# Kernel optimization log

Hardware: AMD Instinct MI355X
Metric: run time of the kernel (lower is better)

Reference implementation:

```python
import jax, jax.numpy as jnp
import numpy as np

EMBED = 1024
HEADS = 16
HEAD_DIM = EMBED // HEADS
HIDDEN = int(EMBED * 4.0)
EPS = 1e-6


def setup_inputs() -> dict:
    key = jax.random.key(0)
    ks = jax.random.split(key, 8)
    s = lambda fan_in: 1.0 / np.sqrt(fan_in)
    x = jax.random.normal(ks[0], (2, 2048, EMBED), dtype=jnp.float32)
    return {
        "x": x,
        "ln1_g": jnp.ones((EMBED,), jnp.float32),
        "ln1_b": jnp.zeros((EMBED,), jnp.float32),
        "w_qkv": jax.random.normal(ks[1], (EMBED, 3 * EMBED), jnp.float32) * s(EMBED),
        "b_qkv": jnp.zeros((3 * EMBED,), jnp.float32),
        "w_proj": jax.random.normal(ks[2], (EMBED, EMBED), jnp.float32) * s(EMBED),
        "b_proj": jnp.zeros((EMBED,), jnp.float32),
        "ln2_g": jnp.ones((EMBED,), jnp.float32),
        "ln2_b": jnp.zeros((EMBED,), jnp.float32),
        "w_fc1": jax.random.normal(ks[3], (EMBED, HIDDEN), jnp.float32) * s(EMBED),
        "b_fc1": jnp.zeros((HIDDEN,), jnp.float32),
        "w_fc2": jax.random.normal(ks[4], (HIDDEN, EMBED), jnp.float32) * s(HIDDEN),
        "b_fc2": jnp.zeros((EMBED,), jnp.float32),
    }


def _layernorm(x, g, b):
    mu = jnp.mean(x, axis=-1, keepdims=True)
    var = jnp.mean(jnp.square(x - mu), axis=-1, keepdims=True)
    return (x - mu) * jax.lax.rsqrt(var + EPS) * g + b


def _attention(x, w_qkv, b_qkv, w_proj, b_proj):
    B, N, C = x.shape
    qkv = x @ w_qkv + b_qkv                      # [B,N,3C]
    qkv = qkv.reshape(B, N, 3, HEADS, HEAD_DIM)
    q, k, v = (qkv[:, :, 0], qkv[:, :, 1], qkv[:, :, 2])  # [B,N,H,Dh]
    scale = HEAD_DIM ** -0.5
    attn = jnp.einsum('bnhd,bmhd->bhnm', q, k) * scale     # [B,H,N,N]
    attn = jax.nn.softmax(attn, axis=-1)
    out = jnp.einsum('bhnm,bmhd->bnhd', attn, v).reshape(B, N, C)
    return out @ w_proj + b_proj


def reference(x, ln1_g, ln1_b, w_qkv, b_qkv, w_proj, b_proj,
              ln2_g, ln2_b, w_fc1, b_fc1, w_fc2, b_fc2):
    x = x + _attention(_layernorm(x, ln1_g, ln1_b), w_qkv, b_qkv, w_proj, b_proj)
    h = _layernorm(x, ln2_g, ln2_b)
    h = jax.nn.gelu(h @ w_fc1 + b_fc1, approximate=False)
    x = x + (h @ w_fc2 + b_fc2)
    return x
```

## Files before the change

kernel.cpp:

```cpp
#include <hip/hip_runtime.h>
#include <hip/hip_bf16.h>
#include <math.h>

typedef __bf16 bf16x8 __attribute__((ext_vector_type(8)));
typedef __bf16 bf16x4 __attribute__((ext_vector_type(4)));
typedef unsigned short u16x8 __attribute__((ext_vector_type(8)));
typedef float f32x4 __attribute__((ext_vector_type(4)));

#define EP_QKV 0
#define EP_GELU 1
#define EP_RES 2

static __device__ __forceinline__ unsigned short f2bf(float x) {
  unsigned int u = __float_as_uint(x);
  unsigned int r = (u + 0x7fffu + ((u >> 16) & 1u)) >> 16;
  return (unsigned short)r;
}

static __device__ __forceinline__ unsigned int pkbf(float lo, float hi) {
  return __builtin_amdgcn_perm(__float_as_uint(hi), __float_as_uint(lo), 0x07060302);
}

static __device__ __forceinline__ void async16(const void* g, void* l) {
  __builtin_amdgcn_global_load_lds((__attribute__((address_space(1))) void*)g,
                                   (__attribute__((address_space(3))) void*)l, 16, 0, 0);
}

__global__ __launch_bounds__(256) void wt_all(
    const float* __restrict__ i0, unsigned short* __restrict__ o0,
    const float* __restrict__ i1, unsigned short* __restrict__ o1,
    const float* __restrict__ i2, unsigned short* __restrict__ o2,
    const float* __restrict__ i3, unsigned short* __restrict__ o3) {
  __shared__ float tile[32][33];
  const int b = blockIdx.x;
  const float* in; unsigned short* out; int K, N, nbx, lb;
  if (b < 3072)      { in = i0; out = o0; K = 1024; N = 3072; nbx = 96;  lb = b; }
  else if (b < 4096) { in = i1; out = o1; K = 1024; N = 1024; nbx = 32;  lb = b - 3072; }
  else if (b < 8192) { in = i2; out = o2; K = 1024; N = 4096; nbx = 128; lb = b - 4096; }
  else               { in = i3; out = o3; K = 4096; N = 1024; nbx = 32;  lb = b - 8192; }
  const int n0 = (lb % nbx) * 32;
  const int k0 = (lb / nbx) * 32;
  const int tx = threadIdx.x;
  const int ty = threadIdx.y;
  #pragma unroll
  for (int i = ty; i < 32; i += 8)
    tile[i][tx] = in[(size_t)(k0 + i) * N + n0 + tx];
  __syncthreads();
  #pragma unroll
  for (int i = ty; i < 32; i += 8)
    out[(size_t)(n0 + i) * K + k0 + tx] = f2bf(tile[tx][i]);
}

__global__ __launch_bounds__(256) void ln_kernel(const float* __restrict__ x,
                                                 const float* __restrict__ g,
                                                 const float* __restrict__ b,
                                                 unsigned short* __restrict__ outp) {
  const int row = blockIdx.x;
  const int tid = threadIdx.x;
  const int wave = tid >> 6, lane = tid & 63;
  const float4 v = ((const float4*)(x + (size_t)row * 1024))[tid];
  float s = v.x + v.y + v.z + v.w;
  #pragma unroll
  for (int i = 1; i < 64; i <<= 1) s += __shfl_xor(s, i);
  __shared__ float red[4];
  if (lane == 0) red[wave] = s;
  __syncthreads();
  const float mean = (red[0] + red[1] + red[2] + red[3]) * (1.f / 1024.f);
  const float dx = v.x - mean, dy = v.y - mean, dz = v.z - mean, dw = v.w - mean;
  float ss = dx * dx + dy * dy + dz * dz + dw * dw;
  #pragma unroll
  for (int i = 1; i < 64; i <<= 1) ss += __shfl_xor(ss, i);
  __syncthreads();
  if (lane == 0) red[wave] = ss;
  __syncthreads();
  const float var = (red[0] + red[1] + red[2] + red[3]) * (1.f / 1024.f);
  const float inv = rsqrtf(var + 1e-6f);
  const float4 gv = ((const float4*)g)[tid];
  const float4 bv = ((const float4*)b)[tid];
  ushort4 o;
  o.x = f2bf(dx * inv * gv.x + bv.x);
  o.y = f2bf(dy * inv * gv.y + bv.y);
  o.z = f2bf(dz * inv * gv.z + bv.z);
  o.w = f2bf(dw * inv * gv.w + bv.w);
  ((ushort4*)(outp + (size_t)row * 1024))[tid] = o;
}

template <int TN, int BK, bool DBUF, int MODE, int MINW>
__global__ __launch_bounds__(256, MINW) void gemm_kernel(
    const unsigned short* __restrict__ A,
    const unsigned short* __restrict__ BT,
    const float* __restrict__ bias,
    int M, int N, int K,
    void* __restrict__ outp, const float* __restrict__ res) {
  constexpr int AM = (TN == 128) ? 4 : 2;
  constexpr int ACH = BK / 16;
  constexpr int BCH = TN * BK / 2048;
  constexpr int CPR = BK / 8;
  constexpr int ABYTES = 256 * BK;
  constexpr int BBYTES = TN * BK * 2;
  constexpr int NBUF = DBUF ? 2 : 1;
  __shared__ __align__(16) char smem[NBUF * (ABYTES + BBYTES)];

  const int tid = threadIdx.x;
  const int wave = tid >> 6, lane = tid & 63;
  const int quad = lane >> 4, l16 = lane & 15;
  const int wm = (TN == 128) ? (wave >> 1) : wave;
  const int wn = (TN == 128) ? (wave & 1) : 0;

  const int nbm = M >> 7, nbn = N / TN;
  const int lin = blockIdx.y * gridDim.x + blockIdx.x;
  const int g = lin & 7, idx = lin >> 3;
  const int gm = nbm >> 2, gn = nbn >> 1;
  const int bm = (g & 3) * gm + (idx % gm);
  const int bn = (g >> 2) * gn + (idx / gm);
  const int row_m = bm * 128, row_n = bn * TN;

  int ar[ACH], ac[ACH];
  #pragma unroll
  for (int i = 0; i < ACH; ++i) {
    const int c = wave * (64 * ACH) + i * 64 + lane;
    ar[i] = c / CPR;
    ac[i] = ((c % CPR) ^ (ar[i] & (CPR - 1))) * 8;
  }
  int br[BCH], bc[BCH];
  #pragma unroll
  for (int i = 0; i < BCH; ++i) {
    const int c = wave * (64 * BCH) + i * 64 + lane;
    br[i] = c / CPR;
    bc[i] = ((c % CPR) ^ (br[i] & (CPR - 1))) * 8;
  }

  const unsigned short* Ag = A + (size_t)row_m * K;
  const unsigned short* Bg = BT + (size_t)row_n * K;

  const f32x4 z = {0.f, 0.f, 0.f, 0.f};
  f32x4 acc[AM][4];
  #pragma unroll
  for (int i = 0; i < AM; ++i)
    #pragma unroll
    for (int j = 0; j < 4; ++j) acc[i][j] = z;

  auto issue = [&](int kt, int b) {
    unsigned short* As = (unsigned short*)(smem + b * ABYTES);
    unsigned short* Bs = (unsigned short*)(smem + NBUF * ABYTES + b * BBYTES);
    #pragma unroll
    for (int i = 0; i < ACH; ++i)
      async16(Ag + (size_t)ar[i] * K + kt + ac[i], As + wave * (ACH * 512) + i * 512);
    #pragma unroll
    for (int i = 0; i < BCH; ++i)
      async16(Bg + (size_t)br[i] * K + kt + bc[i], Bs + wave * (BCH * 512) + i * 512);
  };

  auto computeTile = [&](int b) {
    const unsigned short* As = (const unsigned short*)(smem + b * ABYTES);
    const unsigned short* Bs = (const unsigned short*)(smem + NBUF * ABYTES + b * BBYTES);
    #pragma unroll
    for (int h = 0; h < BK / 32; ++h) {
      bf16x8 af[AM], bfv[4];
      #pragma unroll
      for (int t = 0; t < AM; ++t) {
        const int row = wm * (AM * 16) + t * 16 + l16;
        const int ch = (h * 4 + quad) ^ (row & (CPR - 1));
        af[t] = *(const bf16x8*)(As + row * BK + ch * 8);
      }
      #pragma unroll
      for (int t = 0; t < 4; ++t) {
        const int row = wn * 64 + t * 16 + l16;
        const int ch = (h * 4 + quad) ^ (row & (CPR - 1));
        bfv[t] = *(const bf16x8*)(Bs + row * BK + ch * 8);
      }
      #pragma unroll
      for (int tm = 0; tm < AM; ++tm)
        #pragma unroll
        for (int tn = 0; tn < 4; ++tn)
          acc[tm][tn] = __builtin_amdgcn_mfma_f32_16x16x32_bf16(af[tm], bfv[tn], acc[tm][tn], 0, 0, 0);
    }
  };

  if constexpr (DBUF) {
    issue(0, 0);
    for (int kt = 0; kt < K; kt += BK) {
      const int b = (kt / BK) & 1;
      __syncthreads();
      if (kt + BK < K) issue(kt + BK, b ^ 1);
      computeTile(b);
    }
  } else {
    for (int kt = 0; kt < K; kt += BK) {
      issue(kt, 0);
      __syncthreads();
      computeTile(0);
      __syncthreads();
    }
  }

  #pragma unroll
  for (int tn = 0; tn < 4; ++tn) {
    const int col = row_n + wn * 64 + tn * 16 + l16;
    const float bv = bias[col];
    #pragma unroll
    for (int tm = 0; tm < AM; ++tm) {
      const int rbase = row_m + wm * (AM * 16) + tm * 16 + quad * 4;
      float v[4];
      #pragma unroll
      for (int r = 0; r < 4; ++r) v[r] = acc[tm][tn][r] + bv;
      if constexpr (MODE == EP_QKV) {
        unsigned short* outw = (unsigned short*)outp;
        const int which = col >> 10;
        const int h = (col >> 6) & 15, d = col & 63;
        const int bb = rbase >> 11, n = rbase & 2047;
        const size_t bh = (size_t)(bb * 16 + h);
        if (which == 0) {
          #pragma unroll
          for (int r = 0; r < 4; ++r)
            outw[(bh * 2048 + n + r) * 64 + d] = f2bf(v[r] * 0.18033688011112043f);
        } else if (which == 1) {
          #pragma unroll
          for (int r = 0; r < 4; ++r)
            outw[4194304ull + (bh * 2048 + n + r) * 64 + d] = f2bf(v[r]);
        } else {
          uint2 o;
          o.x = pkbf(v[0], v[1]);
          o.y = pkbf(v[2], v[3]);
          *(uint2*)(outw + 8388608ull + (bh * 64 + d) * 2048 + n) = o;
        }
      } else if constexpr (MODE == EP_GELU) {
        #pragma unroll
        for (int r = 0; r < 4; ++r) {
          const float u = v[r];
          const float c = 1.5957691216f * fmaf(0.044715f * u * u, u, u);
          const float e = __expf(c);
          const float gl = u - __fdividef(u, e + 1.0f);
          ((unsigned short*)outp)[(size_t)(rbase + r) * N + col] = f2bf(gl);
        }
      } else {
        #pragma unroll
        for (int r = 0; r < 4; ++r)
          ((float*)outp)[(size_t)(rbase + r) * N + col] =
              res[(size_t)(rbase + r) * N + col] + v[r];
      }
    }
  }
}

__global__ __launch_bounds__(256, 3) void attn_kernel(
    const unsigned short* __restrict__ Q,
    const unsigned short* __restrict__ Kb,
    const unsigned short* __restrict__ VT,
    unsigned short* __restrict__ outp) {
  __shared__ __align__(16) char smem[49152];
  unsigned short* Ks = (unsigned short*)smem;
  unsigned short* Vs = (unsigned short*)(smem + 32768);

  const int tid = threadIdx.x;
  const int wave = tid >> 6, lane = tid & 63;
  const int quad = lane >> 4, l16 = lane & 15;

  const int lin = blockIdx.y * gridDim.x + blockIdx.x;
  const int g = lin & 7, idx = lin >> 3;
  const int bhi = g * 4 + (idx >> 5);
  const int q0 = (idx & 31) * 64;

  const unsigned short* Qg = Q + ((size_t)bhi * 2048 + q0) * 64;
  const unsigned short* Kg = Kb + (size_t)bhi * 2048 * 64;
  const unsigned short* Vg = VT + (size_t)bhi * 64 * 2048;

  const unsigned short* kp[4];
  const unsigned short* vp[4];
  #pragma unroll
  for (int i = 0; i < 4; ++i) {
    const int c = wave * 256 + i * 64 + lane;
    const int krr = c >> 3, kcc = ((c & 7) ^ (krr & 7)) * 8;
    const int vrr = c >> 4, vcc = ((c & 15) ^ (vrr & 15)) * 8;
    kp[i] = Kg + (size_t)krr * 64 + kcc;
    vp[i] = Vg + (size_t)vrr * 2048 + vcc;
  }

  auto issueK = [&](int b) {
    unsigned short* Kd = Ks + b * 8192;
    #pragma unroll
    for (int i = 0; i < 4; ++i) async16(kp[i], Kd + wave * 2048 + i * 512);
    #pragma unroll
    for (int i = 0; i < 4; ++i) kp[i] += 8192;
  };
  auto issueV = [&]() {
    #pragma unroll
    for (int i = 0; i < 4; ++i) async16(vp[i], Vs + wave * 2048 + i * 512);
    #pragma unroll
    for (int i = 0; i < 4; ++i) vp[i] += 128;
  };

  issueK(0);

  bf16x8 qb[4][2];
  #pragma unroll
  for (int nt = 0; nt < 4; ++nt)
    #pragma unroll
    for (int h = 0; h < 2; ++h)
      qb[nt][h] = *(const bf16x8*)(Qg + (nt * 16 + l16) * 64 + (h * 4 + quad) * 8);

  const f32x4 z = {0.f, 0.f, 0.f, 0.f};
  f32x4 acc[4][4];
  #pragma unroll
  for (int i = 0; i < 4; ++i)
    #pragma unroll
    for (int j = 0; j < 4; ++j) acc[i][j] = z;
  float lsum[4] = {0.f, 0.f, 0.f, 0.f};

  const int rowA = wave * 16 + l16;
  const int rowB = 64 + rowA;
  const int swk = l16 & 7;

  bf16x8 pb[4];
  auto computeQK = [&](int b) {
    const unsigned short* Ksb = Ks + b * 8192;
    f32x4 sA[4], sB[4];
    #pragma unroll
    for (int nt = 0; nt < 4; ++nt) { sA[nt] = z; sB[nt] = z; }
    __builtin_amdgcn_s_setprio(1);
    #pragma unroll
    for (int h = 0; h < 2; ++h) {
      const int ch = (h * 4 + quad) ^ swk;
      bf16x8 kfA = *(const bf16x8*)(Ksb + rowA * 64 + ch * 8);
      bf16x8 kfB = *(const bf16x8*)(Ksb + rowB * 64 + ch * 8);
      #pragma unroll
      for (int nt = 0; nt < 4; ++nt) {
        sA[nt] = __builtin_amdgcn_mfma_f32_16x16x32_bf16(kfA, qb[nt][h], sA[nt], 0, 0, 0);
        sB[nt] = __builtin_amdgcn_mfma_f32_16x16x32_bf16(kfB, qb[nt][h], sB[nt], 0, 0, 0);
      }
    }
    __builtin_amdgcn_s_setprio(0);
    #pragma unroll
    for (int nt = 0; nt < 4; ++nt) {
      union { unsigned int d[4]; bf16x8 b; } cv;
      float pa[4], pv[4];
      float ls = 0.f;
      #pragma unroll
      for (int r = 0; r < 4; ++r) {
        pa[r] = __builtin_amdgcn_exp2f(sA[nt][r]);
        pv[r] = __builtin_amdgcn_exp2f(sB[nt][r]);
        ls += pa[r] + pv[r];
      }
      cv.d[0] = pkbf(pa[0], pa[1]);
      cv.d[1] = pkbf(pa[2], pa[3]);
      cv.d[2] = pkbf(pv[0], pv[1]);
      cv.d[3] = pkbf(pv[2], pv[3]);
      lsum[nt] += ls;
      pb[nt] = cv.b;
    }
  };

  auto computePV = [&]() {
    __builtin_amdgcn_s_setprio(1);
    #pragma unroll
    for (int mt = 0; mt < 4; ++mt) {
      const int d = mt * 16 + l16;
      const int cA = (wave * 2 + (quad >> 1)) ^ (d & 15);
      const int cB = (8 + wave * 2 + (quad >> 1)) ^ (d & 15);
      const int sub = (quad & 1) * 4;
      bf16x4 vA = *(const bf16x4*)(Vs + d * 128 + cA * 8 + sub);
      bf16x4 vB = *(const bf16x4*)(Vs + d * 128 + cB * 8 + sub);
      bf16x8 vf = __builtin_shufflevector(vA, vB, 0, 1, 2, 3, 4, 5, 6, 7);
      #pragma unroll
      for (int nt = 0; nt < 4; ++nt)
        acc[mt][nt] = __builtin_amdgcn_mfma_f32_16x16x32_bf16(vf, pb[nt], acc[mt][nt], 0, 0, 0);
    }
    __builtin_amdgcn_s_setprio(0);
  };

  for (int t = 0; t < 16; ++t) {
    __syncthreads();
    issueV();
    issueK((t + 1) & 1);
    computeQK(t & 1);
    asm volatile("s_waitcnt vmcnt(4) lgkmcnt(0)\n\ts_barrier" ::: "memory");
    computePV();
  }
  __syncthreads();

  float* sc = (float*)smem;
  float* lred = (float*)(smem + 32768);
  #pragma unroll
  for (int nt = 0; nt < 4; ++nt) {
    float ls = lsum[nt];
    ls += __shfl_xor(ls, 16);
    ls += __shfl_xor(ls, 32);
    if (quad == 0) lred[wave * 64 + nt * 16 + l16] = ls;
  }
  if (wave >= 2) {
    float* dst = sc + (wave - 2) * 4096;
    #pragma unroll
    for (int mt = 0; mt < 4; ++mt)
      #pragma unroll
      for (int nt = 0; nt < 4; ++nt)
        *(f32x4*)(dst + (mt * 4 + nt) * 256 + lane * 4) = acc[mt][nt];
  }
  __syncthreads();
  if (wave < 2) {
    const float* src = sc + wave * 4096;
    #pragma unroll
    for (int mt = 0; mt < 4; ++mt)
      #pragma unroll
      for (int nt = 0; nt < 4; ++nt)
        acc[mt][nt] += *(const f32x4*)(src + (mt * 4 + nt) * 256 + lane * 4);
  }
  if (wave == 1) {
    float* dst = sc + 4096;
    #pragma unroll
    for (int mt = 0; mt < 4; ++mt)
      #pragma unroll
      for (int nt = 0; nt < 4; ++nt)
        *(f32x4*)(dst + (mt * 4 + nt) * 256 + lane * 4) = acc[mt][nt];
  }
  __syncthreads();
  if (wave == 0) {
    const float* src = sc + 4096;
    float linv[4];
    #pragma unroll
    for (int nt = 0; nt < 4; ++nt) {
      const int qi = nt * 16 + l16;
      const float l = lred[qi] + lred[64 + qi] + lred[128 + qi] + lred[192 + qi];
      linv[nt] = 1.0f / l;
    }
    const int b = bhi >> 4, h = bhi & 15;
    #pragma unroll
    for (int mt = 0; mt < 4; ++mt)
      #pragma unroll
      for (int nt = 0; nt < 4; ++nt) {
        f32x4 o = acc[mt][nt] + *(const f32x4*)(src + (mt * 4 + nt) * 256 + lane * 4);
        uint2 ov;
        ov.x = pkbf(o[0] * linv[nt], o[1] * linv[nt]);
        ov.y = pkbf(o[2] * linv[nt], o[3] * linv[nt]);
        *(uint2*)(outp + ((size_t)(b * 2048 + q0 + nt * 16 + l16)) * 1024 +
                  h * 64 + mt * 16 + quad * 4) = ov;
      }
  }
}

extern "C" void kernel_launch(void* const* d_in, const int* in_sizes, int n_in,
                              void* d_out, int out_size, void* d_ws, size_t ws_size,
                              hipStream_t stream) {
  (void)in_sizes; (void)n_in; (void)out_size; (void)ws_size;
  const float* x      = (const float*)d_in[0];
  const float* ln1_g  = (const float*)d_in[1];
  const float* ln1_b  = (const float*)d_in[2];
  const float* w_qkv  = (const float*)d_in[3];
  const float* b_qkv  = (const float*)d_in[4];
  const float* w_proj = (const float*)d_in[5];
  const float* b_proj = (const float*)d_in[6];
  const float* ln2_g  = (const float*)d_in[7];
  const float* ln2_b  = (const float*)d_in[8];
  const float* w_fc1  = (const float*)d_in[9];
  const float* b_fc1  = (const float*)d_in[10];
  const float* w_fc2  = (const float*)d_in[11];
  const float* b_fc2  = (const float*)d_in[12];

  char* ws = (char*)d_ws;
  unsigned short* wqkvT  = (unsigned short*)(ws + 0);
  unsigned short* wprojT = (unsigned short*)(ws + 6291456);
  unsigned short* wfc1T  = (unsigned short*)(ws + 8388608);
  unsigned short* wfc2T  = (unsigned short*)(ws + 16777216);
  unsigned short* lnb    = (unsigned short*)(ws + 25165824);
  unsigned short* qkvb   = (unsigned short*)(ws + 33554432);
  unsigned short* attnb  = (unsigned short*)(ws + 58720256);
  float*          x2     = (float*)(ws + 67108864);
  unsigned short* hbuf   = qkvb;

  wt_all<<<12288, dim3(32, 8), 0, stream>>>(w_qkv, wqkvT, w_proj, wprojT,
                                            w_fc1, wfc1T, w_fc2, wfc2T);

  ln_kernel<<<4096, 256, 0, stream>>>(x, ln1_g, ln1_b, lnb);

  gemm_kernel<128, 64, false, EP_QKV, 3><<<dim3(24, 32), 256, 0, stream>>>(
      lnb, wqkvT, b_qkv, 4096, 3072, 1024, (void*)qkvb, nullptr);

  attn_kernel<<<dim3(32, 32), 256, 0, stream>>>(qkvb, qkvb + 4194304, qkvb + 8388608, attnb);

  gemm_kernel<64, 64, true, EP_RES, 2><<<dim3(16, 32), 256, 0, stream>>>(
      attnb, wprojT, b_proj, 4096, 1024, 1024, (void*)x2, x);

  ln_kernel<<<4096, 256, 0, stream>>>(x2, ln2_g, ln2_b, lnb);

  gemm_kernel<128, 64, false, EP_GELU, 3><<<dim3(32, 32), 256, 0, stream>>>(
      lnb, wfc1T, b_fc1, 4096, 4096, 1024, (void*)hbuf, nullptr);

  gemm_kernel<64, 64, true, EP_RES, 2><<<dim3(16, 32), 256, 0, stream>>>(
      hbuf, wfc2T, b_fc2, 4096, 1024, 4096, d_out, x2);
}
```

Baseline: 321.0 us.

## Add 256x256-tile 512-thread GEMM kernel for the FC1 GELU matmul

Result: no change. 319.0 us (-0.6%).

```diff
diff --git a/kernel.cpp b/kernel.cpp
--- a/kernel.cpp
+++ b/kernel.cpp
@@ -243,6 +243,121 @@
   }
 }
 
+template <int MODE>
+__global__ __launch_bounds__(512, 2) void gemm256_kernel(
+    const unsigned short* __restrict__ A,
+    const unsigned short* __restrict__ BT,
+    const float* __restrict__ bias,
+    int M, int N, int K,
+    void* __restrict__ outp, const float* __restrict__ res) {
+  __shared__ __align__(16) char smem[131072];
+
+  const int tid = threadIdx.x;
+  const int wave = tid >> 6, lane = tid & 63;
+  const int quad = lane >> 4, l16 = lane & 15;
+  const int wm = wave >> 2;
+  const int wn = wave & 3;
+
+  const int nbm = M >> 8, nbn = N >> 8;
+  const int lin = blockIdx.y * gridDim.x + blockIdx.x;
+  const int g = lin & 7, idx = lin >> 3;
+  const int gm = nbm >> 2, gn = nbn >> 1;
+  const int bm = (g & 3) * gm + (idx % gm);
+  const int bn = (g >> 2) * gn + (idx / gm);
+  const int row_m = bm * 256, row_n = bn * 256;
+
+  int ar[4], ac[4];
+  #pragma unroll
+  for (int i = 0; i < 4; ++i) {
+    const int c = wave * 256 + i * 64 + lane;
+    const int rr = c >> 3;
+    ar[i] = rr;
+    ac[i] = ((c & 7) ^ (rr & 7)) * 8;
+  }
+
+  const unsigned short* Ag = A + (size_t)row_m * K;
+  const unsigned short* Bg = BT + (size_t)row_n * K;
+
+  const f32x4 z = {0.f, 0.f, 0.f, 0.f};
+  f32x4 acc[8][4];
+  #pragma unroll
+  for (int i = 0; i < 8; ++i)
+    #pragma unroll
+    for (int j = 0; j < 4; ++j) acc[i][j] = z;
+
+  auto issue = [&](int kt, int b) {
+    unsigned short* As = (unsigned short*)(smem + b * 65536);
+    unsigned short* Bs = (unsigned short*)(smem + b * 65536 + 32768);
+    #pragma unroll
+    for (int i = 0; i < 4; ++i)
+      async16(Ag + (size_t)ar[i] * K + kt + ac[i], As + wave * 2048 + i * 512);
+    #pragma unroll
+    for (int i = 0; i < 4; ++i)
+      async16(Bg + (size_t)ar[i] * K + kt + ac[i], Bs + wave * 2048 + i * 512);
+  };
+
+  auto computeTile = [&](int b) {
+    const unsigned short* As = (const unsigned short*)(smem + b * 65536);
+    const unsigned short* Bs = (const unsigned short*)(smem + b * 65536 + 32768);
+    #pragma unroll
+    for (int h = 0; h < 2; ++h) {
+      bf16x8 bfv[4];
+      #pragma unroll
+      for (int t = 0; t < 4; ++t) {
+        const int row = wn * 64 + t * 16 + l16;
+        const int ch = (h * 4 + quad) ^ (row & 7);
+        bfv[t] = *(const bf16x8*)(Bs + row * 64 + ch * 8);
+      }
+      #pragma unroll
+      for (int tm = 0; tm < 8; ++tm) {
+        const int row = wm * 128 + tm * 16 + l16;
+        const int ch = (h * 4 + quad) ^ (row & 7);
+        bf16x8 af = *(const bf16x8*)(As + row * 64 + ch * 8);
+        #pragma unroll
+        for (int tn = 0; tn < 4; ++tn)
+          acc[tm][tn] = __builtin_amdgcn_mfma_f32_16x16x32_bf16(af, bfv[tn], acc[tm][tn], 0, 0, 0);
+      }
+    }
+  };
+
+  issue(0, 0);
+  for (int t = 0; t < 16; ++t) {
+    const int b = t & 1;
+    issue((t + 1) * 64, b ^ 1);
+    asm volatile("s_waitcnt vmcnt(8) lgkmcnt(0)\n\ts_barrier" ::: "memory");
+    computeTile(b);
+    asm volatile("s_waitcnt lgkmcnt(0)\n\ts_barrier" ::: "memory");
+  }
+
+  #pragma unroll
+  for (int tn = 0; tn < 4; ++tn) {
+    const int col = row_n + wn * 64 + tn * 16 + l16;
+    const float bv = bias[col];
+    #pragma unroll
+    for (int tm = 0; tm < 8; ++tm) {
+      const int rbase = row_m + wm * 128 + tm * 16 + quad * 4;
+      float v[4];
+      #pragma unroll
+      for (int r = 0; r < 4; ++r) v[r] = acc[tm][tn][r] + bv;
+      if constexpr (MODE == EP_GELU) {
+        #pragma unroll
+        for (int r = 0; r < 4; ++r) {
+          const float u = v[r];
+          const float c = 1.5957691216f * fmaf(0.044715f * u * u, u, u);
+          const float e = __expf(c);
+          const float gl = u - __fdividef(u, e + 1.0f);
+          ((unsigned short*)outp)[(size_t)(rbase + r) * N + col] = f2bf(gl);
+        }
+      } else {
+        #pragma unroll
+        for (int r = 0; r < 4; ++r)
+          ((float*)outp)[(size_t)(rbase + r) * N + col] =
+              res[(size_t)(rbase + r) * N + col] + v[r];
+      }
+    }
+  }
+}
+
 __global__ __launch_bounds__(256, 3) void attn_kernel(
     const unsigned short* __restrict__ Q,
     const unsigned short* __restrict__ Kb,
@@ -481,7 +596,7 @@
 
   ln_kernel<<<4096, 256, 0, stream>>>(x2, ln2_g, ln2_b, lnb);
 
-  gemm_kernel<128, 64, false, EP_GELU, 3><<<dim3(32, 32), 256, 0, stream>>>(
+  gemm256_kernel<EP_GELU><<<dim3(16, 16), 512, 0, stream>>>(
       lnb, wfc1T, b_fc1, 4096, 4096, 1024, (void*)hbuf, nullptr);
 
   gemm_kernel<64, 64, true, EP_RES, 2><<<dim3(16, 32), 256, 0, stream>>>(
```
